# Kernel optimization log

Hardware: AMD Instinct MI355X
Metric: run time of the kernel (lower is better)

## Reference

```python
import jax, jax.numpy as jnp
import numpy as np

RADIUS = 0.5
NEG_INF = -jnp.inf


def setup_inputs() -> dict:
    key = jax.random.key(0)
    ks = jax.random.split(key, 10)
    N_q, N_o, pos_dim, latent_dim = 2048, 2048, 3, 64
    enc_dim = 3 * pos_dim  # q_pos, o_pos, rel
    inp = {
        "h_obs": jax.random.normal(ks[0], (N_o, latent_dim), dtype=jnp.float32),
        "x_obs": jax.random.normal(ks[1], (N_o, latent_dim), dtype=jnp.float32),
        "pos_obs": jax.random.uniform(ks[2], (N_o, pos_dim), dtype=jnp.float32),
        "pos_query": jax.random.uniform(ks[3], (N_q, pos_dim), dtype=jnp.float32),
        # kernel_mlp: Linear(enc_dim->latent) + ReLU + Linear(latent->1)
        "W1": jax.random.normal(ks[4], (enc_dim, latent_dim), dtype=jnp.float32) / np.sqrt(enc_dim),
        "b1": jnp.zeros((latent_dim,), dtype=jnp.float32),
        "W2": jax.random.normal(ks[5], (latent_dim, 1), dtype=jnp.float32) / np.sqrt(latent_dim),
        "b2": jnp.zeros((1,), dtype=jnp.float32),
        # value_proj: Linear(latent->latent)
        "Wv": jax.random.normal(ks[6], (latent_dim, latent_dim), dtype=jnp.float32) / np.sqrt(latent_dim),
        "bv": jnp.zeros((latent_dim,), dtype=jnp.float32),
    }
    return inp


def reference(h_obs, x_obs, pos_obs, pos_query, W1, b1, W2, b2, Wv, bv):
    # rel: [N_q, N_o, pos_dim]
    rel = pos_query[:, None, :] - pos_obs[None, :, :]
    N_q, N_o, _ = rel.shape
    pos_q_exp = jnp.broadcast_to(pos_query[:, None, :], rel.shape)
    pos_o_exp = jnp.broadcast_to(pos_obs[None, :, :], rel.shape)
    kernel_input = jnp.concatenate([pos_q_exp, pos_o_exp, rel], axis=-1)  # [N_q, N_o, 3*pos_dim]
    # small pointwise MLP over all pairs
    hidden = jax.nn.relu(jnp.einsum('qoe,el->qol', kernel_input, W1) + b1)  # [N_q, N_o, latent]
    logits = jnp.einsum('qol,lk->qok', hidden, W2)[..., 0] + b2[0]          # [N_q, N_o]
    # radius mask
    dist = jnp.linalg.norm(rel, axis=-1)
    logits = jnp.where(dist > RADIUS, NEG_INF, logits)
    # softmax over observations (dim=1)
    weights = jax.nn.softmax(logits, axis=1)  # [N_q, N_o]
    v = h_obs @ Wv + bv                        # [N_o, latent]
    h_query = weights @ v                      # [N_q, latent]
    return h_query
```

## Files before the change

### kernel.cpp

```cpp
#include <hip/hip_runtime.h>

#define NQ 2048
#define NO 2048
#define NOC 32

constexpr size_t OFF_PH = 0;
constexpr size_t OFF_PS = (size_t)NOC * NQ * 64;

__global__ __launch_bounds__(256, 2) void gano_prep(
    const float* __restrict__ h_obs,
    const float* __restrict__ Wv,
    float* __restrict__ V)
{
    __shared__ __align__(16) float wv[64 * 64];
    const int tid  = threadIdx.x;
    const int lane = tid & 63;
    const int wave = tid >> 6;
    {
        const float4* src = (const float4*)Wv;
        float4* dst = (float4*)wv;
#pragma unroll
        for (int k = 0; k < 4; ++k) dst[tid + k * 256] = src[tid + k * 256];
    }
    __syncthreads();
    const int o = blockIdx.x * 4 + wave;
    const float4* hp = (const float4*)(h_obs + (size_t)o * 64);
    float a0 = 0.f, a1 = 0.f, a2 = 0.f, a3 = 0.f;
#pragma unroll
    for (int kb = 0; kb < 16; ++kb) {
        float4 h4 = hp[kb];
        a0 += h4.x * wv[(kb * 4 + 0) * 64 + lane];
        a1 += h4.y * wv[(kb * 4 + 1) * 64 + lane];
        a2 += h4.z * wv[(kb * 4 + 2) * 64 + lane];
        a3 += h4.w * wv[(kb * 4 + 3) * 64 + lane];
    }
    V[(size_t)o * 64 + lane] = (a0 + a1) + (a2 + a3);
}

__global__ __launch_bounds__(256, 4) void gano_main(
    const float* __restrict__ V,
    const float* __restrict__ pos_obs,
    const float* __restrict__ pos_query,
    const float* __restrict__ W1,
    const float* __restrict__ b1,
    const float* __restrict__ W2,
    float* __restrict__ Ph,
    float* __restrict__ Ps)
{
    __shared__ __align__(16) float tl[64 * 68];
    __shared__ __align__(16) float ue[16 * 64 * 4];
    __shared__ float w1q[3 * 64];
    __shared__ float w1o[3 * 64];
    __shared__ float b1l[64];
    __shared__ __align__(16) float w2l[64];
    __shared__ float po[3 * 64];
    __shared__ float sbuf[4 * 64];

    const int tid  = threadIdx.x;
    const int lane = tid & 63;
    const int wave = __builtin_amdgcn_readfirstlane(tid >> 6);
    const int qg = blockIdx.x >> 5;
    const int oc = blockIdx.x & 31;
    const int obase = oc * 64;
    const int q = qg * 64 + lane;

    if (tid < 64) {
        float w6 = W1[6 * 64 + tid], w7 = W1[7 * 64 + tid], w8 = W1[8 * 64 + tid];
        w1q[0 * 64 + tid] = W1[0 * 64 + tid] + w6;
        w1q[1 * 64 + tid] = W1[1 * 64 + tid] + w7;
        w1q[2 * 64 + tid] = W1[2 * 64 + tid] + w8;
        w1o[0 * 64 + tid] = W1[3 * 64 + tid] - w6;
        w1o[1 * 64 + tid] = W1[4 * 64 + tid] - w7;
        w1o[2 * 64 + tid] = W1[5 * 64 + tid] - w8;
        b1l[tid] = b1[tid];
        w2l[tid] = W2[tid];
    }
    float pq0 = pos_query[q * 3 + 0];
    float pq1 = pos_query[q * 3 + 1];
    float pq2 = pos_query[q * 3 + 2];
    float po0 = pos_obs[(obase + lane) * 3 + 0];
    float po1 = pos_obs[(obase + lane) * 3 + 1];
    float po2 = pos_obs[(obase + lane) * 3 + 2];
    if (wave == 0) { po[lane] = po0; po[64 + lane] = po1; po[128 + lane] = po2; }
    __syncthreads();

#pragma unroll
    for (int j = 0; j < 16; ++j) {
        int l = wave * 16 + j;
        tl[l * 68 + lane] = po0 * w1o[l] + po1 * w1o[64 + l] + po2 * w1o[128 + l];
    }
#pragma unroll
    for (int k = 0; k < 4; ++k) {
        int lb = wave * 4 + k;
        float4 uv;
        {
            int l = lb * 4;
            uv.x = b1l[l+0] + pq0 * w1q[l+0] + pq1 * w1q[64 + l+0] + pq2 * w1q[128 + l+0];
            uv.y = b1l[l+1] + pq0 * w1q[l+1] + pq1 * w1q[64 + l+1] + pq2 * w1q[128 + l+1];
            uv.z = b1l[l+2] + pq0 * w1q[l+2] + pq1 * w1q[64 + l+2] + pq2 * w1q[128 + l+2];
            uv.w = b1l[l+3] + pq0 * w1q[l+3] + pq1 * w1q[64 + l+3] + pq2 * w1q[128 + l+3];
        }
        *(float4*)(ue + (size_t)(lb * 64 + lane) * 4) = uv;
    }
    __syncthreads();

    float lg[16];
#pragma unroll
    for (int o = 0; o < 16; ++o) lg[o] = 0.f;
    const int ow = wave * 16;
#pragma unroll
    for (int lb = 0; lb < 16; ++lb) {
        float4 u4 = *(const float4*)(ue + (size_t)(lb * 64 + lane) * 4);
        float4 w4 = *(const float4*)(w2l + lb * 4);
#pragma unroll
        for (int dl = 0; dl < 4; ++dl) {
            const int l = lb * 4 + dl;
            const float4* tr = (const float4*)(tl + l * 68 + ow);
            float ul = (dl == 0) ? u4.x : (dl == 1) ? u4.y : (dl == 2) ? u4.z : u4.w;
            float wl = (dl == 0) ? w4.x : (dl == 1) ? w4.y : (dl == 2) ? w4.z : w4.w;
#pragma unroll
            for (int j = 0; j < 4; ++j) {
                float4 t4 = tr[j];
                lg[4 * j + 0] += wl * fmaxf(ul + t4.x, 0.f);
                lg[4 * j + 1] += wl * fmaxf(ul + t4.y, 0.f);
                lg[4 * j + 2] += wl * fmaxf(ul + t4.z, 0.f);
                lg[4 * j + 3] += wl * fmaxf(ul + t4.w, 0.f);
            }
        }
    }
    float e[16], spart = 0.f;
#pragma unroll
    for (int o = 0; o < 16; ++o) {
        float d0 = pq0 - po[ow + o];
        float d1 = pq1 - po[64 + ow + o];
        float d2 = pq2 - po[128 + ow + o];
        float dd = d0 * d0 + d1 * d1 + d2 * d2;
        float ev = (dd > 0.25f) ? 0.f : __expf(lg[o]);
        e[o] = ev; spart += ev;
    }
    __syncthreads();
#pragma unroll
    for (int o = 0; o < 16; ++o) ue[(size_t)(ow + o) * 64 + lane] = e[o];
    sbuf[wave * 64 + lane] = spart;
    __syncthreads();

    float h0 = 0.f, h1 = 0.f, h2 = 0.f, h3 = 0.f, h4 = 0.f, h5 = 0.f, h6 = 0.f, h7 = 0.f;
    float h8 = 0.f, h9 = 0.f, hA = 0.f, hB = 0.f, hC = 0.f, hD = 0.f, hE = 0.f, hF = 0.f;
    const float* vb = V + (size_t)obase * 64 + ow;
#pragma unroll 4
    for (int o = 0; o < 64; ++o) {
        float eo = ue[(size_t)o * 64 + lane];
        const float4* vr = (const float4*)(vb + (size_t)o * 64);
        float4 v0 = vr[0], v1 = vr[1], v2 = vr[2], v3 = vr[3];
        h0 += eo * v0.x; h1 += eo * v0.y; h2 += eo * v0.z; h3 += eo * v0.w;
        h4 += eo * v1.x; h5 += eo * v1.y; h6 += eo * v1.z; h7 += eo * v1.w;
        h8 += eo * v2.x; h9 += eo * v2.y; hA += eo * v2.z; hB += eo * v2.w;
        hC += eo * v3.x; hD += eo * v3.y; hE += eo * v3.z; hF += eo * v3.w;
    }

    float* hp = Ph + ((size_t)oc * NQ + (size_t)qg * 64 + lane) * 64 + ow;
    ((float4*)hp)[0] = make_float4(h0, h1, h2, h3);
    ((float4*)hp)[1] = make_float4(h4, h5, h6, h7);
    ((float4*)hp)[2] = make_float4(h8, h9, hA, hB);
    ((float4*)hp)[3] = make_float4(hC, hD, hE, hF);
    if (wave == 0) {
        float s = sbuf[lane] + sbuf[64 + lane] + sbuf[128 + lane] + sbuf[192 + lane];
        Ps[(size_t)oc * NQ + (size_t)qg * 64 + lane] = s;
    }
}

__global__ __launch_bounds__(256) void gano_comb(
    const float* __restrict__ Ph,
    const float* __restrict__ Ps,
    const float* __restrict__ bv,
    float* __restrict__ out)
{
    const int tid = threadIdx.x;
    const int l = tid & 63;
    const int qi = tid >> 6;
    const int q = blockIdx.x * 4 + qi;
    float hs = 0.f, ss = 0.f;
#pragma unroll
    for (int c = 0; c < NOC; ++c) {
        hs += Ph[((size_t)c * NQ + q) * 64 + l];
        ss += Ps[(size_t)c * NQ + q];
    }
    out[(size_t)q * 64 + l] = hs / ss + bv[l];
}

extern "C" void kernel_launch(void* const* d_in, const int* in_sizes, int n_in,
                              void* d_out, int out_size, void* d_ws, size_t ws_size,
                              hipStream_t stream) {
    const float* h_obs     = (const float*)d_in[0];
    const float* pos_obs   = (const float*)d_in[2];
    const float* pos_query = (const float*)d_in[3];
    const float* W1        = (const float*)d_in[4];
    const float* b1        = (const float*)d_in[5];
    const float* W2        = (const float*)d_in[6];
    const float* Wv        = (const float*)d_in[8];
    const float* bv        = (const float*)d_in[9];
    float* ws  = (float*)d_ws;
    float* out = (float*)d_out;

    gano_prep<<<dim3(NO / 4), dim3(256), 0, stream>>>(h_obs, Wv, out);
    gano_main<<<dim3(1024), dim3(256), 0, stream>>>(out, pos_obs, pos_query, W1, b1, W2,
                                                    ws + OFF_PH, ws + OFF_PS);
    gano_comb<<<dim3(NQ / 4), dim3(256), 0, stream>>>(ws + OFF_PH, ws + OFF_PS, bv, out);
}
```

Before: 109.0 us.

## Apply value projection after softmax aggregation to drop the prep kernel

```diff
diff --git a/kernel.cpp b/kernel.cpp
--- a/kernel.cpp
+++ b/kernel.cpp
@@ -7,38 +7,8 @@
 constexpr size_t OFF_PH = 0;
 constexpr size_t OFF_PS = (size_t)NOC * NQ * 64;
 
-__global__ __launch_bounds__(256, 2) void gano_prep(
+__global__ __launch_bounds__(256, 4) void gano_main(
     const float* __restrict__ h_obs,
-    const float* __restrict__ Wv,
-    float* __restrict__ V)
-{
-    __shared__ __align__(16) float wv[64 * 64];
-    const int tid  = threadIdx.x;
-    const int lane = tid & 63;
-    const int wave = tid >> 6;
-    {
-        const float4* src = (const float4*)Wv;
-        float4* dst = (float4*)wv;
-#pragma unroll
-        for (int k = 0; k < 4; ++k) dst[tid + k * 256] = src[tid + k * 256];
-    }
-    __syncthreads();
-    const int o = blockIdx.x * 4 + wave;
-    const float4* hp = (const float4*)(h_obs + (size_t)o * 64);
-    float a0 = 0.f, a1 = 0.f, a2 = 0.f, a3 = 0.f;
-#pragma unroll
-    for (int kb = 0; kb < 16; ++kb) {
-        float4 h4 = hp[kb];
-        a0 += h4.x * wv[(kb * 4 + 0) * 64 + lane];
-        a1 += h4.y * wv[(kb * 4 + 1) * 64 + lane];
-        a2 += h4.z * wv[(kb * 4 + 2) * 64 + lane];
-        a3 += h4.w * wv[(kb * 4 + 3) * 64 + lane];
-    }
-    V[(size_t)o * 64 + lane] = (a0 + a1) + (a2 + a3);
-}
-
-__global__ __launch_bounds__(256, 4) void gano_main(
-    const float* __restrict__ V,
     const float* __restrict__ pos_obs,
     const float* __restrict__ pos_query,
     const float* __restrict__ W1,
@@ -146,7 +116,7 @@
 
     float h0 = 0.f, h1 = 0.f, h2 = 0.f, h3 = 0.f, h4 = 0.f, h5 = 0.f, h6 = 0.f, h7 = 0.f;
     float h8 = 0.f, h9 = 0.f, hA = 0.f, hB = 0.f, hC = 0.f, hD = 0.f, hE = 0.f, hF = 0.f;
-    const float* vb = V + (size_t)obase * 64 + ow;
+    const float* vb = h_obs + (size_t)obase * 64 + ow;
 #pragma unroll 4
     for (int o = 0; o < 64; ++o) {
         float eo = ue[(size_t)o * 64 + lane];
@@ -169,23 +139,52 @@
     }
 }
 
-__global__ __launch_bounds__(256) void gano_comb(
+__global__ __launch_bounds__(256, 2) void gano_comb(
     const float* __restrict__ Ph,
     const float* __restrict__ Ps,
+    const float* __restrict__ Wv,
     const float* __restrict__ bv,
     float* __restrict__ out)
 {
-    const int tid = threadIdx.x;
-    const int l = tid & 63;
-    const int qi = tid >> 6;
-    const int q = blockIdx.x * 4 + qi;
-    float hs = 0.f, ss = 0.f;
-#pragma unroll
-    for (int c = 0; c < NOC; ++c) {
-        hs += Ph[((size_t)c * NQ + q) * 64 + l];
-        ss += Ps[(size_t)c * NQ + q];
-    }
-    out[(size_t)q * 64 + l] = hs / ss + bv[l];
+    __shared__ __align__(16) float wv[64 * 64];
+    __shared__ __align__(16) float g[4 * 68];
+    const int tid  = threadIdx.x;
+    const int lane = tid & 63;
+    const int wave = tid >> 6;
+    const int q0 = blockIdx.x * 4;
+    {
+        const float4* src = (const float4*)Wv;
+        float4* dst = (float4*)wv;
+#pragma unroll
+        for (int k = 0; k < 4; ++k) dst[tid + k * 256] = src[tid + k * 256];
+    }
+    {
+        const int qi = wave, k = lane;
+        float acc = 0.f;
+#pragma unroll
+        for (int c = 0; c < NOC; ++c)
+            acc += Ph[((size_t)c * NQ + q0 + qi) * 64 + k];
+        g[qi * 68 + k] = acc;
+        if (k == 0) {
+            float ss = 0.f;
+#pragma unroll
+            for (int c = 0; c < NOC; ++c) ss += Ps[(size_t)c * NQ + q0 + qi];
+            g[qi * 68 + 64] = ss;
+        }
+    }
+    __syncthreads();
+    const float* gq = g + wave * 68;
+    float inv = 1.0f / gq[64];
+    float a0 = 0.f, a1 = 0.f, a2 = 0.f, a3 = 0.f;
+#pragma unroll
+    for (int kb = 0; kb < 16; ++kb) {
+        float4 g4 = *(const float4*)(gq + kb * 4);
+        a0 += g4.x * wv[(kb * 4 + 0) * 64 + lane];
+        a1 += g4.y * wv[(kb * 4 + 1) * 64 + lane];
+        a2 += g4.z * wv[(kb * 4 + 2) * 64 + lane];
+        a3 += g4.w * wv[(kb * 4 + 3) * 64 + lane];
+    }
+    out[(size_t)(q0 + wave) * 64 + lane] = ((a0 + a1) + (a2 + a3)) * inv + bv[lane];
 }
 
 extern "C" void kernel_launch(void* const* d_in, const int* in_sizes, int n_in,
@@ -202,8 +201,7 @@
     float* ws  = (float*)d_ws;
     float* out = (float*)d_out;
 
-    gano_prep<<<dim3(NO / 4), dim3(256), 0, stream>>>(h_obs, Wv, out);
-    gano_main<<<dim3(1024), dim3(256), 0, stream>>>(out, pos_obs, pos_query, W1, b1, W2,
+    gano_main<<<dim3(1024), dim3(256), 0, stream>>>(h_obs, pos_obs, pos_query, W1, b1, W2,
                                                     ws + OFF_PH, ws + OFF_PS);
-    gano_comb<<<dim3(NQ / 4), dim3(256), 0, stream>>>(ws + OFF_PH, ws + OFF_PS, bv, out);
+    gano_comb<<<dim3(NQ / 4), dim3(256), 0, stream>>>(ws + OFF_PH, ws + OFF_PS, Wv, bv, out);
 }
```

Measured after the change: 108.2 us. About the same (-0.7%).
